# Optimization experiments

Measured on AMD Instinct MI355X. Metric: run time of the kernel, lower is better.

The kernel has to match this reference:

```python
import jax, jax.numpy as jnp
import numpy as np

V_IPC, N_ROLES, D = 50000, 16, 256
B, L = 2048, 64
F_BIB, H1, H2, D_OUT = 512, 1024, 1024, 512
N_EXP, N_CLS = 8, 10
LN_EPS = 1e-5


def setup_inputs() -> dict:
    key = jax.random.key(0)
    ks = jax.random.split(key, 24)
    s = 0.05
    ipc_emb = jax.random.normal(ks[0], (V_IPC, D), jnp.float32) * s
    ipc_emb = ipc_emb.at[0].set(0.0)  # padding_idx=0
    role_emb = jax.random.normal(ks[1], (N_ROLES, D), jnp.float32) * s
    role_emb = role_emb.at[0].set(0.0)
    inp = {
        "ipc_indices": jax.random.randint(ks[2], (B, L), 0, V_IPC),
        "role_indices": jax.random.randint(ks[3], (B, L), 0, N_ROLES),
        "bibliometric_features": jax.random.normal(ks[4], (B, F_BIB), jnp.float32),
        "ipc_padding_mask": jax.random.randint(ks[5], (B, L), 0, 2).astype(jnp.int32),
        "top_k": 2,
        "ipc_emb": ipc_emb,
        "role_emb": role_emb,
        "Wq": jax.random.normal(ks[6], (D, D), jnp.float32) * s,
        "bq": jnp.zeros((D,), jnp.float32),
        "Wk": jax.random.normal(ks[7], (D, D), jnp.float32) * s,
        "bk": jnp.zeros((D,), jnp.float32),
        "Wv": jax.random.normal(ks[8], (D, D), jnp.float32) * s,
        "bv": jnp.zeros((D,), jnp.float32),
        "global_context": jax.random.normal(ks[9], (D,), jnp.float32) * s,
        "ln_g": jnp.ones((D,), jnp.float32),
        "ln_b": jnp.zeros((D,), jnp.float32),
        "gate_W": jax.random.normal(ks[10], (D, N_EXP), jnp.float32) * s,
        "gate_b": jnp.zeros((N_EXP,), jnp.float32),
        "expert_biases": jnp.zeros((N_EXP,), jnp.float32),
        "W1": jax.random.normal(ks[11], (N_EXP, F_BIB, H1), jnp.float32) * s,
        "b1": jnp.zeros((N_EXP, H1), jnp.float32),
        "W2": jax.random.normal(ks[12], (N_EXP, H1, H2), jnp.float32) * s,
        "b2": jnp.zeros((N_EXP, H2), jnp.float32),
        "W3": jax.random.normal(ks[13], (N_EXP, H2, D_OUT), jnp.float32) * s,
        "b3": jnp.zeros((N_EXP, D_OUT), jnp.float32),
        "head_W": jax.random.normal(ks[14], (D_OUT, N_CLS), jnp.float32) * s,
        "head_b": jnp.zeros((N_CLS,), jnp.float32),
    }
    return inp


def reference(ipc_indices, role_indices, bibliometric_features, ipc_padding_mask, top_k,
              ipc_emb, role_emb, Wq, bq, Wk, bk, Wv, bv, global_context, ln_g, ln_b,
              gate_W, gate_b, expert_biases, W1, b1, W2, b2, W3, b3, head_W, head_b):
    # embeddings + role combine  -> [B, L, D]
    x = ipc_emb[ipc_indices] + role_emb[role_indices]
    # attention pooling with a global learned query (same query for every batch row)
    keys = x @ Wk + bk                                  # [B, L, D]
    values = x @ Wv + bv                                # [B, L, D]
    q = global_context @ Wq + bq                        # [D]
    scores = jnp.einsum('d,bld->bl', q, keys)           # [B, L]
    scores = jnp.where(ipc_padding_mask == 0, -1e9, scores)
    attn = jax.nn.softmax(scores, axis=-1)              # [B, L]
    pooled = jnp.einsum('bl,bld->bd', attn, values)     # [B, D]
    mu = pooled.mean(-1, keepdims=True)
    var = ((pooled - mu) ** 2).mean(-1, keepdims=True)
    router_in = (pooled - mu) / jnp.sqrt(var + LN_EPS) * ln_g + ln_b
    # router: select with biased scores, gate with unbiased scores
    affinity = router_in @ gate_W + gate_b              # [B, E]
    sel_scores = affinity + expert_biases
    _, idx = jax.lax.top_k(sel_scores, top_k)           # [B, K]
    gw = jax.nn.softmax(jnp.take_along_axis(affinity, idx, axis=-1), axis=-1)  # [B, K]
    # dense all-expert MLP (reference form of masked per-expert loop)
    h = jax.nn.relu(jnp.einsum('bi,eih->ebh', bibliometric_features, W1) + b1[:, None, :])
    h = jax.nn.relu(jnp.einsum('ebh,ehj->ebj', h, W2) + b2[:, None, :])
    eo = jnp.einsum('ebj,ejo->ebo', h, W3) + b3[:, None, :]  # [E, B, O]
    # gather each token's top-k expert outputs and combine
    bidx = jnp.arange(idx.shape[0])[:, None]            # [B, 1]
    sel_out = eo[idx, bidx]                             # [B, K, O]
    moe_out = jnp.einsum('bk,bko->bo', gw, sel_out)     # [B, O]
    logits = moe_out @ head_W + head_b                  # [B, n_classes]
    return logits, idx
```

## Files before the change

### kernel.cpp

```cpp
#include <hip/hip_runtime.h>
#include <hip/hip_bf16.h>
#include <math.h>


#define LN_EPS 1e-5f

typedef __bf16 bf16_t;
typedef __bf16 bf16x8 __attribute__((ext_vector_type(8)));
typedef float f32x4 __attribute__((ext_vector_type(4)));

struct f4x2 { float4 a, b; };
__device__ __forceinline__ f4x2 ldA8(const float* p) {
  f4x2 v; v.a = *(const float4*)p; v.b = *(const float4*)(p + 4); return v;
}
__device__ __forceinline__ bf16x8 cvt8(const f4x2& v) {
  bf16x8 o;
  o[0] = (bf16_t)v.a.x; o[1] = (bf16_t)v.a.y; o[2] = (bf16_t)v.a.z; o[3] = (bf16_t)v.a.w;
  o[4] = (bf16_t)v.b.x; o[5] = (bf16_t)v.b.y; o[6] = (bf16_t)v.b.z; o[7] = (bf16_t)v.b.w;
  return o;
}

__global__ __launch_bounds__(256)
void prep_kq_kernel(const float* __restrict__ Wq, const float* __restrict__ bq,
                    const float* __restrict__ Wk, const float* __restrict__ bk,
                    const float* __restrict__ gc, float* __restrict__ kq_out,
                    int* __restrict__ done_ctr) {
  __shared__ float q[256];
  __shared__ float red[4];
  const int t = threadIdx.x, bi = blockIdx.x;
  if (bi == 0 && t == 0) *done_ctr = 0;
  float s = bq[t];
  for (int d = 0; d < 256; d++) s += gc[d] * Wq[d * 256 + t];
  q[t] = s;
  __syncthreads();
  const int rl = t >> 5, sl = t & 31;
  const int r = bi * 8 + rl;
  float p = 0.f;
#pragma unroll
  for (int i = 0; i < 8; i++) { const int d = sl + 32 * i; p += Wk[r * 256 + d] * q[d]; }
#pragma unroll
  for (int o = 16; o > 0; o >>= 1) p += __shfl_down(p, o, 32);
  if (sl == 0) kq_out[r] = p;
  if (bi == 0) {
    float z2 = q[t] * bk[t];
    const int lane = t & 63, wave = t >> 6;
#pragma unroll
    for (int o = 32; o > 0; o >>= 1) z2 += __shfl_down(z2, o);
    if (lane == 0) red[wave] = z2;
    __syncthreads();
    if (t == 0) kq_out[256] = red[0] + red[1] + red[2] + red[3];
  }
}

__global__ __launch_bounds__(256, 8)
void xbar_transpose(const float* __restrict__ W1, const float* __restrict__ W2,
                    const float* __restrict__ W3, bf16_t* __restrict__ B1,
                    bf16_t* __restrict__ B2, bf16_t* __restrict__ B3,
                    const int* __restrict__ ipc_idx, const int* __restrict__ role_idx,
                    const int* __restrict__ maskp,
                    const float* __restrict__ ipc_emb, const float* __restrict__ role_emb,
                    const float* __restrict__ kq_qbk, float* __restrict__ xbar_g) {
  __shared__ __align__(16) float smem[4480];
  __shared__ int s_ii[64], s_ri[64], s_mk[64];
  const int bid = blockIdx.x;
  const int t = threadIdx.x, lane = t & 63;

  if (bid < 2048) {
    const int b = bid, wave = t >> 6;
    float* sred = smem;
    float* scores_s = smem + 4352;
    float* attn_s = smem + 4416;
    const float4 kq = *(const float4*)(kq_qbk + lane * 4);
    const float qbk = kq_qbk[256];
    if (t < 64) {
      const int mk = maskp[b * 64 + t];
      s_mk[t] = mk;
      s_ii[t] = mk ? ipc_idx[b * 64 + t] : 0;
      s_ri[t] = mk ? role_idx[b * 64 + t] : 0;
    }
    __syncthreads();
#pragma unroll
    for (int i = 0; i < 16; i++) {
      const int row = wave * 16 + i;
      const int ii = s_ii[row], ri = s_ri[row];
      const float4 xe = *(const float4*)(ipc_emb + (size_t)ii * 256 + lane * 4);
      const float4 re = *(const float4*)(role_emb + (size_t)ri * 256 + lane * 4);
      sred[(wave * 64 + lane) * 17 + i] =
          (xe.x + re.x) * kq.x + (xe.y + re.y) * kq.y +
          (xe.z + re.z) * kq.z + (xe.w + re.w) * kq.w;
    }
    __syncthreads();
    {
      const int i_r = lane & 15, g = lane >> 4;
      float s = 0.f;
#pragma unroll
      for (int j = 0; j < 16; j++) s += sred[(wave * 64 + g * 16 + j) * 17 + i_r];
      s += __shfl_xor(s, 16);
      s += __shfl_xor(s, 32);
      if (lane < 16)
        scores_s[wave * 16 + lane] = s_mk[wave * 16 + lane] ? (s + qbk) : -1e9f;
    }
    __syncthreads();
    if (wave == 0) {
      const float sv = scores_s[lane];
      float m = sv;
#pragma unroll
      for (int o = 32; o > 0; o >>= 1) m = fmaxf(m, __shfl_xor(m, o));
      const float ev = expf(sv - m);
      float sum = ev;
#pragma unroll
      for (int o = 32; o > 0; o >>= 1) sum += __shfl_xor(sum, o);
      attn_s[lane] = ev / sum;
    }
    __syncthreads();
    float p0 = 0.f, p1 = 0.f, p2 = 0.f, p3 = 0.f;
#pragma unroll
    for (int i = 0; i < 16; i++) {
      const int row = wave * 16 + i;
      const int ii = s_ii[row], ri = s_ri[row];
      const float a = attn_s[row];
      const float4 xe = *(const float4*)(ipc_emb + (size_t)ii * 256 + lane * 4);
      const float4 re = *(const float4*)(role_emb + (size_t)ri * 256 + lane * 4);
      p0 += a * (xe.x + re.x); p1 += a * (xe.y + re.y);
      p2 += a * (xe.z + re.z); p3 += a * (xe.w + re.w);
    }
    __syncthreads();
    *(float4*)&smem[wave * 256 + lane * 4] = make_float4(p0, p1, p2, p3);
    __syncthreads();
    xbar_g[(size_t)b * 256 + t] = smem[t] + smem[256 + t] + smem[512 + t] + smem[768 + t];
    return;
  }

  const int bid2 = bid - 2048;
  const float* W; bf16_t* Bft; int K, N, e, n0, k0;
  if (bid2 < 1024) {
    W = W1; Bft = B1; K = 512; N = 1024;
    e = bid2 >> 7; const int r = bid2 & 127;
    n0 = (r & 15) * 64; k0 = (r >> 4) * 64;
  } else if (bid2 < 3072) {
    W = W2; Bft = B2; K = 1024; N = 1024;
    const int q = bid2 - 1024; e = q >> 8; const int r = q & 255;
    n0 = (r & 15) * 64; k0 = (r >> 4) * 64;
  } else {
    W = W3; Bft = B3; K = 1024; N = 512;
    const int q = bid2 - 3072; e = q >> 7; const int r = q & 127;
    n0 = (r & 7) * 64; k0 = (r >> 3) * 64;
  }
  float (*tile)[65] = (float(*)[65])smem;
  const float* Wp = W + (size_t)e * K * N;
  bf16_t* Bp = Bft + (size_t)e * N * K;
  const int tq = t & 15, th = t >> 4;
#pragma unroll
  for (int i = 0; i < 4; i++) {
    const int row = th + 16 * i;
    *(float4*)&tile[row][tq * 4] = *(const float4*)(Wp + (size_t)(k0 + row) * N + n0 + tq * 4);
  }
  __syncthreads();
  const int sub = t >> 6;
  const int nk = K >> 5;
#pragma unroll
  for (int it = 0; it < 2; it++) {
    const int fid = sub + it * 4;
    const int ntl = fid & 3, ktl = fid >> 2;
    const int n_l = ntl * 16 + (lane & 15);
    const int k_l = ktl * 32 + (lane >> 4) * 8;
    bf16x8 o;
#pragma unroll
    for (int j = 0; j < 8; j++) o[j] = (bf16_t)tile[k_l + j][n_l];
    const size_t idx = ((((size_t)(n0 >> 4) + ntl) * nk + (k0 >> 5) + ktl) * 64 + lane) * 8;
    *(bf16x8*)(Bp + idx) = o;
  }
}

__global__ __launch_bounds__(256)
void pool_kernel(const float* __restrict__ xbar_g, const float* __restrict__ Wv,
                 const float* __restrict__ bvec,
                 const float* __restrict__ ln_g, const float* __restrict__ ln_b,
                 const float* __restrict__ gate_W, const float* __restrict__ gate_b,
                 const float* __restrict__ expert_biases,
                 float* __restrict__ out_idx_f, int* __restrict__ ws_idx,
                 float* __restrict__ ws_gw, int* __restrict__ done_ctr,
                 int* __restrict__ list_token, int* __restrict__ a_of,
                 int* __restrict__ offsets_g) {
  const int rb = blockIdx.x * 8;
  __shared__ __align__(16) float xs[8][256];
  __shared__ __align__(16) float pp[4][8][256];
  __shared__ int is_last;
  const int t = threadIdx.x, wave = t >> 6, lane = t & 63;
  for (int i = t; i < 512; i += 256)
    ((float4*)xs)[i] = ((const float4*)(xbar_g + (size_t)rb * 256))[i];
  __syncthreads();
  f32x4 acc[8];
#pragma unroll
  for (int r = 0; r < 8; r++) acc[r] = (f32x4){0.f, 0.f, 0.f, 0.f};
  const int dbase = wave * 64;
  for (int dd = 0; dd < 64; dd += 4) {
    float4 xr[8];
#pragma unroll
    for (int r = 0; r < 8; r++) xr[r] = *(const float4*)&xs[r][dbase + dd];
#pragma unroll
    for (int j = 0; j < 4; j++) {
      const float4 wv = *(const float4*)(Wv + (size_t)(dbase + dd + j) * 256 + lane * 4);
#pragma unroll
      for (int r = 0; r < 8; r++) {
        const float xv = (&xr[r].x)[j];
        acc[r][0] += xv * wv.x; acc[r][1] += xv * wv.y;
        acc[r][2] += xv * wv.z; acc[r][3] += xv * wv.w;
      }
    }
  }
#pragma unroll
  for (int r = 0; r < 8; r++) *(f32x4*)&pp[wave][r][lane * 4] = acc[r];
  __syncthreads();
  const float4 bvv = *(const float4*)(bvec + lane * 4);
  const float4 lg = *(const float4*)(ln_g + lane * 4);
  const float4 lb = *(const float4*)(ln_b + lane * 4);
#pragma unroll
  for (int rr = 0; rr < 2; rr++) {
    const int r = wave * 2 + rr;
    f32x4 v = *(const f32x4*)&pp[0][r][lane * 4];
#pragma unroll
    for (int w2 = 1; w2 < 4; w2++) {
      const f32x4 qv = *(const f32x4*)&pp[w2][r][lane * 4];
      v[0] += qv[0]; v[1] += qv[1]; v[2] += qv[2]; v[3] += qv[3];
    }
    v[0] += bvv.x; v[1] += bvv.y; v[2] += bvv.z; v[3] += bvv.w;
    float s1 = v[0] + v[1] + v[2] + v[3];
#pragma unroll
    for (int o = 32; o > 0; o >>= 1) s1 += __shfl_xor(s1, o);
    const float mu = s1 * (1.f / 256.f);
    const float4 df = make_float4(v[0] - mu, v[1] - mu, v[2] - mu, v[3] - mu);
    float s2 = df.x * df.x + df.y * df.y + df.z * df.z + df.w * df.w;
#pragma unroll
    for (int o = 32; o > 0; o >>= 1) s2 += __shfl_xor(s2, o);
    const float inv = 1.f / sqrtf(s2 * (1.f / 256.f) + LN_EPS);
    f32x4 rv;
    rv[0] = df.x * inv * lg.x + lb.x; rv[1] = df.y * inv * lg.y + lb.y;
    rv[2] = df.z * inv * lg.z + lb.z; rv[3] = df.w * inv * lg.w + lb.w;
    f32x4 pa = {0.f, 0.f, 0.f, 0.f}, pb = {0.f, 0.f, 0.f, 0.f};
#pragma unroll
    for (int k = 0; k < 4; k++) {
      const int d = lane * 4 + k;
      const f32x4 g0 = *(const f32x4*)(gate_W + d * 8);
      const f32x4 g1 = *(const f32x4*)(gate_W + d * 8 + 4);
      pa += rv[k] * g0;
      pb += rv[k] * g1;
    }
#pragma unroll
    for (int o = 32; o > 0; o >>= 1) {
      pa[0] += __shfl_down(pa[0], o); pa[1] += __shfl_down(pa[1], o);
      pa[2] += __shfl_down(pa[2], o); pa[3] += __shfl_down(pa[3], o);
      pb[0] += __shfl_down(pb[0], o); pb[1] += __shfl_down(pb[1], o);
      pb[2] += __shfl_down(pb[2], o); pb[3] += __shfl_down(pb[3], o);
    }
    if (lane == 0) {
      float aff[8];
#pragma unroll
      for (int j = 0; j < 4; j++) { aff[j] = pa[j] + gate_b[j]; aff[4 + j] = pb[j] + gate_b[4 + j]; }
      float b0 = -1e30f; int i0 = 0;
#pragma unroll
      for (int j = 0; j < 8; j++) {
        const float s = aff[j] + expert_biases[j];
        if (s > b0) { b0 = s; i0 = j; }
      }
      float b1v = -1e30f; int i1 = 0;
#pragma unroll
      for (int j = 0; j < 8; j++) {
        const float s = aff[j] + expert_biases[j];
        if (j != i0 && s > b1v) { b1v = s; i1 = j; }
      }
      const float a0 = aff[i0], a1 = aff[i1];
      const float m = fmaxf(a0, a1);
      const float e0 = expf(a0 - m), e1 = expf(a1 - m);
      const float invs = 1.f / (e0 + e1);
      const int bg = rb + r;
      ws_idx[bg * 2] = i0; ws_idx[bg * 2 + 1] = i1;
      ws_gw[bg * 2] = e0 * invs; ws_gw[bg * 2 + 1] = e1 * invs;
      out_idx_f[bg * 2] = (float)i0; out_idx_f[bg * 2 + 1] = (float)i1;
    }
  }
  __syncthreads();
  if (t == 0) {
    __threadfence();
    const int prev = atomicAdd(done_ctr, 1);
    is_last = (prev == (int)gridDim.x - 1);
  }
  __syncthreads();
  if (is_last) {
    __threadfence();
    __shared__ int cnt[8]; __shared__ int offp[9]; __shared__ int fill[8];
    if (t < 8) cnt[t] = 0;
    __syncthreads();
    for (int a = t; a < 4096; a += 256) atomicAdd(&cnt[ws_idx[a]], 1);
    __syncthreads();
    if (t == 0) {
      offp[0] = 0;
      for (int e = 0; e < 8; e++) offp[e + 1] = offp[e] + ((cnt[e] + 63) & ~63);
    }
    __syncthreads();
    if (t < 8) fill[t] = offp[t];
    if (t < 9) offsets_g[t] = offp[t];
    for (int a = t; a < 4608; a += 256) list_token[a] = 0;
    __syncthreads();
    for (int a = t; a < 4096; a += 256) {
      const int e = ws_idx[a];
      const int pos = atomicAdd(&fill[e], 1);
      list_token[pos] = a >> 1;
      a_of[a] = pos;
    }
  }
}

template <int NT, bool RELU>
__global__ __launch_bounds__(256)
void expert_gemm_g1(const float* __restrict__ bib, const int* __restrict__ list_token,
                    const bf16_t* __restrict__ Bft, const float* __restrict__ bias,
                    bf16_t* __restrict__ C, const int* __restrict__ offsets) {
  constexpr int K = 512, nk = K / 32;
  const int e = blockIdx.z;
  const int seg_hi = offsets[e + 1];
  const int blk_row = offsets[e] + blockIdx.y * 128;
  if (blk_row >= seg_hi) return;
  const int wave = threadIdx.x >> 6, lane = threadIdx.x & 63;
  const int row0 = blk_row + wave * 32;
  if (row0 >= seg_hi) return;
  const int n0 = blockIdx.x * 64;
  const int tok0 = list_token[row0 + (lane & 15)];
  const int tok1 = list_token[row0 + 16 + (lane & 15)];
  const float* Ap0 = bib + (size_t)tok0 * 512 + (lane >> 4) * 8;
  const float* Ap1 = bib + (size_t)tok1 * 512 + (lane >> 4) * 8;
  const bf16_t* Bp = Bft + (size_t)e * NT * K + ((size_t)(n0 >> 4) * nk * 512 + lane * 8);
  f32x4 acc[2][4];
#pragma unroll
  for (int i = 0; i < 2; i++)
#pragma unroll
    for (int j = 0; j < 4; j++) acc[i][j] = (f32x4){0.f, 0.f, 0.f, 0.f};
  f4x2 aS[2][2]; bf16x8 bX[2][4];
  aS[0][0] = ldA8(Ap0); aS[0][1] = ldA8(Ap1);
#pragma unroll
  for (int ni = 0; ni < 4; ni++) bX[0][ni] = *(const bf16x8*)(Bp + (size_t)ni * nk * 512);
#pragma unroll
  for (int kt = 0; kt < nk; kt++) {
    const int cur = kt & 1, nxt = cur ^ 1;
    if (kt + 1 < nk) {
      aS[nxt][0] = ldA8(Ap0 + (kt + 1) * 32);
      aS[nxt][1] = ldA8(Ap1 + (kt + 1) * 32);
#pragma unroll
      for (int ni = 0; ni < 4; ni++)
        bX[nxt][ni] = *(const bf16x8*)(Bp + ((size_t)ni * nk + kt + 1) * 512);
    }
    const bf16x8 a0 = cvt8(aS[cur][0]), a1 = cvt8(aS[cur][1]);
#pragma unroll
    for (int ni = 0; ni < 4; ni++) {
      acc[0][ni] = __builtin_amdgcn_mfma_f32_16x16x32_bf16(a0, bX[cur][ni], acc[0][ni], 0, 0, 0);
      acc[1][ni] = __builtin_amdgcn_mfma_f32_16x16x32_bf16(a1, bX[cur][ni], acc[1][ni], 0, 0, 0);
    }
  }
  const int fr = lane & 15, q = lane >> 4;
#pragma unroll
  for (int ni = 0; ni < 4; ni++) {
    const int col = n0 + ni * 16 + fr;
    const float bv = bias[e * NT + col];
#pragma unroll
    for (int mi = 0; mi < 2; mi++) {
#pragma unroll
      for (int r = 0; r < 4; r++) {
        const int row = row0 + mi * 16 + q * 4 + r;
        float v = acc[mi][ni][r] + bv;
        if (RELU) v = fmaxf(v, 0.f);
        C[(size_t)row * NT + col] = (bf16_t)v;
      }
    }
  }
}

template <int K, int NT, bool RELU, typename OUT_T>
__global__ __launch_bounds__(256)
void expert_gemm_ft(const bf16_t* __restrict__ A, const bf16_t* __restrict__ Bft,
                    const float* __restrict__ bias, OUT_T* __restrict__ C,
                    const int* __restrict__ offsets) {
  constexpr int nk = K / 32;
  const int e = blockIdx.z;
  const int seg_hi = offsets[e + 1];
  const int blk_row = offsets[e] + blockIdx.y * 128;
  if (blk_row >= seg_hi) return;
  const int wave = threadIdx.x >> 6, lane = threadIdx.x & 63;
  const int row0 = blk_row + wave * 32;
  if (row0 >= seg_hi) return;
  const int n0 = blockIdx.x * 64;
  const bf16_t* Ap = A + (size_t)(row0 + (lane & 15)) * K + ((lane >> 4) * 8);
  const bf16_t* Bp = Bft + (size_t)e * NT * K + ((size_t)(n0 >> 4) * nk * 512 + lane * 8);
  f32x4 acc[2][4];
#pragma unroll
  for (int i = 0; i < 2; i++)
#pragma unroll
    for (int j = 0; j < 4; j++) acc[i][j] = (f32x4){0.f, 0.f, 0.f, 0.f};
  bf16x8 aX[2][2], bX[2][4];
#pragma unroll
  for (int mi = 0; mi < 2; mi++) aX[0][mi] = *(const bf16x8*)(Ap + mi * 16 * K);
#pragma unroll
  for (int ni = 0; ni < 4; ni++) bX[0][ni] = *(const bf16x8*)(Bp + (size_t)ni * nk * 512);
#pragma unroll
  for (int kt = 0; kt < nk; kt++) {
    const int cur = kt & 1, nxt = cur ^ 1;
    if (kt + 1 < nk) {
#pragma unroll
      for (int mi = 0; mi < 2; mi++)
        aX[nxt][mi] = *(const bf16x8*)(Ap + mi * 16 * K + (kt + 1) * 32);
#pragma unroll
      for (int ni = 0; ni < 4; ni++)
        bX[nxt][ni] = *(const bf16x8*)(Bp + ((size_t)ni * nk + kt + 1) * 512);
    }
#pragma unroll
    for (int mi = 0; mi < 2; mi++)
#pragma unroll
      for (int ni = 0; ni < 4; ni++)
        acc[mi][ni] = __builtin_amdgcn_mfma_f32_16x16x32_bf16(aX[cur][mi], bX[cur][ni], acc[mi][ni], 0, 0, 0);
  }
  const int fr = lane & 15, q = lane >> 4;
#pragma unroll
  for (int ni = 0; ni < 4; ni++) {
    const int col = n0 + ni * 16 + fr;
    const float bv = bias[e * NT + col];
#pragma unroll
    for (int mi = 0; mi < 2; mi++) {
#pragma unroll
      for (int r = 0; r < 4; r++) {
        const int row = row0 + mi * 16 + q * 4 + r;
        float v = acc[mi][ni][r] + bv;
        if (RELU) v = fmaxf(v, 0.f);
        C[(size_t)row * NT + col] = (OUT_T)v;
      }
    }
  }
}

__global__ __launch_bounds__(256)
void head_kernel(const float* __restrict__ O, const int* __restrict__ a_of,
                 const float* __restrict__ ws_gw, const float* __restrict__ head_W,
                 const float* __restrict__ head_b, float* __restrict__ out) {
  const int b = blockIdx.x, t = threadIdx.x;
  __shared__ float m[512];
  const int a0 = a_of[b * 2], a1 = a_of[b * 2 + 1];
  const float g0 = ws_gw[b * 2], g1 = ws_gw[b * 2 + 1];
  for (int d = t; d < 512; d += 256)
    m[d] = g0 * O[(size_t)a0 * 512 + d] + g1 * O[(size_t)a1 * 512 + d];
  __syncthreads();
  if (t < 160) {
    const int c = t >> 4, ch = t & 15;
    float p = 0.f;
#pragma unroll
    for (int i = 0; i < 32; i++) {
      const int d = i * 16 + ch;
      p += m[d] * head_W[d * 10 + c];
    }
#pragma unroll
    for (int o = 8; o > 0; o >>= 1) p += __shfl_down(p, o, 16);
    if (ch == 0) out[b * 10 + c] = p + head_b[c];
  }
}

extern "C" void kernel_launch(void* const* d_in, const int* in_sizes, int n_in,
                              void* d_out, int out_size, void* d_ws, size_t ws_size,
                              hipStream_t stream) {
  const int* ipc_idx = (const int*)d_in[0];
  const int* role_idx = (const int*)d_in[1];
  const float* bib = (const float*)d_in[2];
  const int* maskp = (const int*)d_in[3];
  const float* ipc_emb = (const float*)d_in[5];
  const float* role_emb = (const float*)d_in[6];
  const float* Wq = (const float*)d_in[7];
  const float* bq = (const float*)d_in[8];
  const float* Wk = (const float*)d_in[9];
  const float* bk = (const float*)d_in[10];
  const float* Wv = (const float*)d_in[11];
  const float* bv = (const float*)d_in[12];
  const float* gc = (const float*)d_in[13];
  const float* ln_g = (const float*)d_in[14];
  const float* ln_b = (const float*)d_in[15];
  const float* gate_W = (const float*)d_in[16];
  const float* gate_b = (const float*)d_in[17];
  const float* exp_b = (const float*)d_in[18];
  const float* W1 = (const float*)d_in[19];
  const float* b1 = (const float*)d_in[20];
  const float* W2 = (const float*)d_in[21];
  const float* b2 = (const float*)d_in[22];
  const float* W3 = (const float*)d_in[23];
  const float* b3 = (const float*)d_in[24];
  const float* head_W = (const float*)d_in[25];
  const float* head_b = (const float*)d_in[26];

  char* ws = (char*)d_ws;
  size_t off = 0;
  auto alloc = [&](size_t bytes) -> char* {
    char* p = ws + off;
    off += (bytes + 255) & ~(size_t)255;
    return p;
  };
  float* kq_qbk = (float*)alloc(257 * 4);
  float* xbar_g = (float*)alloc((size_t)2048 * 256 * 4);
  int* ws_idx = (int*)alloc(4096 * 4);
  float* ws_gw = (float*)alloc(4096 * 4);
  int* list_tok = (int*)alloc(4608 * 4);
  int* a_of = (int*)alloc(4096 * 4);
  int* offs = (int*)alloc(9 * 4);
  int* done_ctr = (int*)alloc(4);
  bf16_t* W1t = (bf16_t*)alloc((size_t)8 * 1024 * 512 * 2);
  bf16_t* W2t = (bf16_t*)alloc((size_t)8 * 1024 * 1024 * 2);
  bf16_t* W3t = (bf16_t*)alloc((size_t)8 * 512 * 1024 * 2);
  bf16_t* H1c = (bf16_t*)alloc((size_t)4608 * 1024 * 2);
  bf16_t* H2c = (bf16_t*)alloc((size_t)4608 * 1024 * 2);
  float* Oc = (float*)alloc((size_t)4608 * 512 * 4);
  (void)in_sizes; (void)n_in; (void)out_size; (void)ws_size;

  float* out_logits = (float*)d_out;
  float* out_idx = (float*)d_out + 20480;

  prep_kq_kernel<<<32, 256, 0, stream>>>(Wq, bq, Wk, bk, gc, kq_qbk, done_ctr);
  xbar_transpose<<<6144, 256, 0, stream>>>(W1, W2, W3, W1t, W2t, W3t,
                                           ipc_idx, role_idx, maskp,
                                           ipc_emb, role_emb, kq_qbk, xbar_g);
  pool_kernel<<<256, 256, 0, stream>>>(xbar_g, Wv, bv, ln_g, ln_b, gate_W, gate_b,
                                       exp_b, out_idx, ws_idx, ws_gw,
                                       done_ctr, list_tok, a_of, offs);
  expert_gemm_g1<1024, true><<<dim3(16, 36, 8), 256, 0, stream>>>(bib, list_tok, W1t, b1, H1c, offs);
  expert_gemm_ft<1024, 1024, true, bf16_t><<<dim3(16, 36, 8), 256, 0, stream>>>(H1c, W2t, b2, H2c, offs);
  expert_gemm_ft<1024, 512, false, float><<<dim3(8, 36, 8), 256, 0, stream>>>(H2c, W3t, b3, Oc, offs);
  head_kernel<<<2048, 256, 0, stream>>>(Oc, a_of, ws_gw, head_W, head_b, out_logits);
}
```

Measured before the change: 365.8 us.

## Fold head projection into W3 so the last expert GEMM outputs ten logits

Precomputes W3·head_W and b3·head_W per expert (padded to 16 columns, stored as bf16 in MFMA fragment layout). The third expert GEMM therefore produces 16 columns instead of 512, and the head kernel becomes a tiny gated combine. This removes most of the layer-3 GEMM FLOPs, the large fp32 Oc buffer and the W3 transpose. Separately, the pooling blocks now load mask and index values straight into registers with vector loads instead of staging them in shared memory. The trade-off is extra rounding, since the folded weights are cast to bf16, and a serial per-class reduction inside the prep blocks.

```diff
diff --git a/kernel.cpp b/kernel.cpp
--- a/kernel.cpp
+++ b/kernel.cpp
@@ -52,16 +52,17 @@
   }
 }
 
-__global__ __launch_bounds__(256, 8)
+__global__ __launch_bounds__(256)
 void xbar_transpose(const float* __restrict__ W1, const float* __restrict__ W2,
                     const float* __restrict__ W3, bf16_t* __restrict__ B1,
-                    bf16_t* __restrict__ B2, bf16_t* __restrict__ B3,
+                    bf16_t* __restrict__ B2, bf16_t* __restrict__ B3h,
+                    float* __restrict__ b3h_g,
+                    const float* __restrict__ b3, const float* __restrict__ head_W,
                     const int* __restrict__ ipc_idx, const int* __restrict__ role_idx,
                     const int* __restrict__ maskp,
                     const float* __restrict__ ipc_emb, const float* __restrict__ role_emb,
                     const float* __restrict__ kq_qbk, float* __restrict__ xbar_g) {
   __shared__ __align__(16) float smem[4480];
-  __shared__ int s_ii[64], s_ri[64], s_mk[64];
   const int bid = blockIdx.x;
   const int t = threadIdx.x, lane = t & 63;
 
@@ -72,17 +73,19 @@
     float* attn_s = smem + 4416;
     const float4 kq = *(const float4*)(kq_qbk + lane * 4);
     const float qbk = kq_qbk[256];
-    if (t < 64) {
-      const int mk = maskp[b * 64 + t];
-      s_mk[t] = mk;
-      s_ii[t] = mk ? ipc_idx[b * 64 + t] : 0;
-      s_ri[t] = mk ? role_idx[b * 64 + t] : 0;
-    }
-    __syncthreads();
+    const int rbase = b * 64 + wave * 16;
+    int4 m4[4], i4[4], r4[4];
+#pragma unroll
+    for (int j = 0; j < 4; j++) {
+      m4[j] = *(const int4*)(maskp + rbase + j * 4);
+      i4[j] = *(const int4*)(ipc_idx + rbase + j * 4);
+      r4[j] = *(const int4*)(role_idx + rbase + j * 4);
+    }
 #pragma unroll
     for (int i = 0; i < 16; i++) {
-      const int row = wave * 16 + i;
-      const int ii = s_ii[row], ri = s_ri[row];
+      const int mki = (&m4[i / 4].x)[i % 4];
+      const int ii = mki ? (&i4[i / 4].x)[i % 4] : 0;
+      const int ri = mki ? (&r4[i / 4].x)[i % 4] : 0;
       const float4 xe = *(const float4*)(ipc_emb + (size_t)ii * 256 + lane * 4);
       const float4 re = *(const float4*)(role_emb + (size_t)ri * 256 + lane * 4);
       sred[(wave * 64 + lane) * 17 + i] =
@@ -97,8 +100,8 @@
       for (int j = 0; j < 16; j++) s += sred[(wave * 64 + g * 16 + j) * 17 + i_r];
       s += __shfl_xor(s, 16);
       s += __shfl_xor(s, 32);
-      if (lane < 16)
-        scores_s[wave * 16 + lane] = s_mk[wave * 16 + lane] ? (s + qbk) : -1e9f;
+      const int mval = (&m4[i_r / 4].x)[i_r % 4];
+      if (lane < 16) scores_s[wave * 16 + lane] = mval ? (s + qbk) : -1e9f;
     }
     __syncthreads();
     if (wave == 0) {
@@ -116,9 +119,10 @@
     float p0 = 0.f, p1 = 0.f, p2 = 0.f, p3 = 0.f;
 #pragma unroll
     for (int i = 0; i < 16; i++) {
-      const int row = wave * 16 + i;
-      const int ii = s_ii[row], ri = s_ri[row];
-      const float a = attn_s[row];
+      const int mki = (&m4[i / 4].x)[i % 4];
+      const int ii = mki ? (&i4[i / 4].x)[i % 4] : 0;
+      const int ri = mki ? (&r4[i / 4].x)[i % 4] : 0;
+      const float a = attn_s[wave * 16 + i];
       const float4 xe = *(const float4*)(ipc_emb + (size_t)ii * 256 + lane * 4);
       const float4 re = *(const float4*)(role_emb + (size_t)ri * 256 + lane * 4);
       p0 += a * (xe.x + re.x); p1 += a * (xe.y + re.y);
@@ -132,19 +136,60 @@
   }
 
   const int bid2 = bid - 2048;
+  if (bid2 >= 3072) {
+    const int q = bid2 - 3072;
+    const int e = q >> 5, kt = q & 31;
+    const int wave = t >> 6;
+    float* w3h_s = smem;
+    for (int i = t; i < 32 * 16; i += 256) w3h_s[i] = 0.f;
+    __syncthreads();
+    const int ob = lane * 8;
+#pragma unroll
+    for (int r = 0; r < 8; r++) {
+      const int kl = wave * 8 + r;
+      const int k = kt * 32 + kl;
+      const f4x2 wv = ldA8(W3 + ((size_t)e * 1024 + k) * 512 + ob);
+      for (int c = 0; c < 10; c++) {
+        float p = wv.a.x * head_W[(ob + 0) * 10 + c] + wv.a.y * head_W[(ob + 1) * 10 + c] +
+                  wv.a.z * head_W[(ob + 2) * 10 + c] + wv.a.w * head_W[(ob + 3) * 10 + c] +
+                  wv.b.x * head_W[(ob + 4) * 10 + c] + wv.b.y * head_W[(ob + 5) * 10 + c] +
+                  wv.b.z * head_W[(ob + 6) * 10 + c] + wv.b.w * head_W[(ob + 7) * 10 + c];
+#pragma unroll
+        for (int o = 32; o > 0; o >>= 1) p += __shfl_down(p, o);
+        if (lane == 0) w3h_s[kl * 16 + c] = p;
+      }
+    }
+    __syncthreads();
+    if (wave == 0) {
+      bf16x8 o8;
+      const int n_l = lane & 15, k_l = (lane >> 4) * 8;
+#pragma unroll
+      for (int j = 0; j < 8; j++) o8[j] = (bf16_t)w3h_s[(k_l + j) * 16 + n_l];
+      *(bf16x8*)(B3h + (size_t)e * 16 * 1024 + ((size_t)kt * 64 + lane) * 8) = o8;
+    }
+    if (kt == 0 && wave == 1) {
+      for (int c = 0; c < 10; c++) {
+        float p = 0.f;
+#pragma unroll
+        for (int j = 0; j < 8; j++) p += b3[e * 512 + ob + j] * head_W[(ob + j) * 10 + c];
+#pragma unroll
+        for (int o = 32; o > 0; o >>= 1) p += __shfl_down(p, o);
+        if (lane == 0) b3h_g[e * 16 + c] = p;
+      }
+      if (lane >= 10 && lane < 16) b3h_g[e * 16 + lane] = 0.f;
+    }
+    return;
+  }
+
   const float* W; bf16_t* Bft; int K, N, e, n0, k0;
   if (bid2 < 1024) {
     W = W1; Bft = B1; K = 512; N = 1024;
     e = bid2 >> 7; const int r = bid2 & 127;
     n0 = (r & 15) * 64; k0 = (r >> 4) * 64;
-  } else if (bid2 < 3072) {
+  } else {
     W = W2; Bft = B2; K = 1024; N = 1024;
     const int q = bid2 - 1024; e = q >> 8; const int r = q & 255;
     n0 = (r & 15) * 64; k0 = (r >> 4) * 64;
-  } else {
-    W = W3; Bft = B3; K = 1024; N = 512;
-    const int q = bid2 - 3072; e = q >> 7; const int r = q & 127;
-    n0 = (r & 7) * 64; k0 = (r >> 3) * 64;
   }
   float (*tile)[65] = (float(*)[65])smem;
   const float* Wp = W + (size_t)e * K * N;
@@ -374,7 +419,7 @@
   }
 }
 
-template <int K, int NT, bool RELU, typename OUT_T>
+template <int K, int NT, int NFRAG, bool RELU, typename OUT_T>
 __global__ __launch_bounds__(256)
 void expert_gemm_ft(const bf16_t* __restrict__ A, const bf16_t* __restrict__ Bft,
                     const float* __restrict__ bias, OUT_T* __restrict__ C,
@@ -387,19 +432,19 @@
   const int wave = threadIdx.x >> 6, lane = threadIdx.x & 63;
   const int row0 = blk_row + wave * 32;
   if (row0 >= seg_hi) return;
-  const int n0 = blockIdx.x * 64;
+  const int n0 = blockIdx.x * (16 * NFRAG);
   const bf16_t* Ap = A + (size_t)(row0 + (lane & 15)) * K + ((lane >> 4) * 8);
   const bf16_t* Bp = Bft + (size_t)e * NT * K + ((size_t)(n0 >> 4) * nk * 512 + lane * 8);
-  f32x4 acc[2][4];
+  f32x4 acc[2][NFRAG];
 #pragma unroll
   for (int i = 0; i < 2; i++)
 #pragma unroll
-    for (int j = 0; j < 4; j++) acc[i][j] = (f32x4){0.f, 0.f, 0.f, 0.f};
-  bf16x8 aX[2][2], bX[2][4];
+    for (int j = 0; j < NFRAG; j++) acc[i][j] = (f32x4){0.f, 0.f, 0.f, 0.f};
+  bf16x8 aX[2][2], bX[2][NFRAG];
 #pragma unroll
   for (int mi = 0; mi < 2; mi++) aX[0][mi] = *(const bf16x8*)(Ap + mi * 16 * K);
 #pragma unroll
-  for (int ni = 0; ni < 4; ni++) bX[0][ni] = *(const bf16x8*)(Bp + (size_t)ni * nk * 512);
+  for (int ni = 0; ni < NFRAG; ni++) bX[0][ni] = *(const bf16x8*)(Bp + (size_t)ni * nk * 512);
 #pragma unroll
   for (int kt = 0; kt < nk; kt++) {
     const int cur = kt & 1, nxt = cur ^ 1;
@@ -408,18 +453,18 @@
       for (int mi = 0; mi < 2; mi++)
         aX[nxt][mi] = *(const bf16x8*)(Ap + mi * 16 * K + (kt + 1) * 32);
 #pragma unroll
-      for (int ni = 0; ni < 4; ni++)
+      for (int ni = 0; ni < NFRAG; ni++)
         bX[nxt][ni] = *(const bf16x8*)(Bp + ((size_t)ni * nk + kt + 1) * 512);
     }
 #pragma unroll
     for (int mi = 0; mi < 2; mi++)
 #pragma unroll
-      for (int ni = 0; ni < 4; ni++)
+      for (int ni = 0; ni < NFRAG; ni++)
         acc[mi][ni] = __builtin_amdgcn_mfma_f32_16x16x32_bf16(aX[cur][mi], bX[cur][ni], acc[mi][ni], 0, 0, 0);
   }
   const int fr = lane & 15, q = lane >> 4;
 #pragma unroll
-  for (int ni = 0; ni < 4; ni++) {
+  for (int ni = 0; ni < NFRAG; ni++) {
     const int col = n0 + ni * 16 + fr;
     const float bv = bias[e * NT + col];
 #pragma unroll
@@ -436,28 +481,15 @@
 }
 
 __global__ __launch_bounds__(256)
-void head_kernel(const float* __restrict__ O, const int* __restrict__ a_of,
-                 const float* __restrict__ ws_gw, const float* __restrict__ head_W,
-                 const float* __restrict__ head_b, float* __restrict__ out) {
-  const int b = blockIdx.x, t = threadIdx.x;
-  __shared__ float m[512];
+void head_small(const float* __restrict__ OcH, const int* __restrict__ a_of,
+                const float* __restrict__ ws_gw, const float* __restrict__ head_b,
+                float* __restrict__ out) {
+  const int tid = blockIdx.x * 256 + threadIdx.x;
+  if (tid >= 20480) return;
+  const int b = tid / 10, c = tid - b * 10;
   const int a0 = a_of[b * 2], a1 = a_of[b * 2 + 1];
   const float g0 = ws_gw[b * 2], g1 = ws_gw[b * 2 + 1];
-  for (int d = t; d < 512; d += 256)
-    m[d] = g0 * O[(size_t)a0 * 512 + d] + g1 * O[(size_t)a1 * 512 + d];
-  __syncthreads();
-  if (t < 160) {
-    const int c = t >> 4, ch = t & 15;
-    float p = 0.f;
-#pragma unroll
-    for (int i = 0; i < 32; i++) {
-      const int d = i * 16 + ch;
-      p += m[d] * head_W[d * 10 + c];
-    }
-#pragma unroll
-    for (int o = 8; o > 0; o >>= 1) p += __shfl_down(p, o, 16);
-    if (ch == 0) out[b * 10 + c] = p + head_b[c];
-  }
+  out[tid] = g0 * OcH[(size_t)a0 * 16 + c] + g1 * OcH[(size_t)a1 * 16 + c] + head_b[c];
 }
 
 extern "C" void kernel_launch(void* const* d_in, const int* in_sizes, int n_in,
@@ -505,26 +537,28 @@
   int* a_of = (int*)alloc(4096 * 4);
   int* offs = (int*)alloc(9 * 4);
   int* done_ctr = (int*)alloc(4);
+  float* b3h = (float*)alloc(8 * 16 * 4);
   bf16_t* W1t = (bf16_t*)alloc((size_t)8 * 1024 * 512 * 2);
   bf16_t* W2t = (bf16_t*)alloc((size_t)8 * 1024 * 1024 * 2);
-  bf16_t* W3t = (bf16_t*)alloc((size_t)8 * 512 * 1024 * 2);
+  bf16_t* B3h = (bf16_t*)alloc((size_t)8 * 16 * 1024 * 2);
   bf16_t* H1c = (bf16_t*)alloc((size_t)4608 * 1024 * 2);
   bf16_t* H2c = (bf16_t*)alloc((size_t)4608 * 1024 * 2);
-  float* Oc = (float*)alloc((size_t)4608 * 512 * 4);
+  float* OcH = (float*)alloc((size_t)4608 * 16 * 4);
   (void)in_sizes; (void)n_in; (void)out_size; (void)ws_size;
 
   float* out_logits = (float*)d_out;
   float* out_idx = (float*)d_out + 20480;
 
   prep_kq_kernel<<<32, 256, 0, stream>>>(Wq, bq, Wk, bk, gc, kq_qbk, done_ctr);
-  xbar_transpose<<<6144, 256, 0, stream>>>(W1, W2, W3, W1t, W2t, W3t,
+  xbar_transpose<<<5376, 256, 0, stream>>>(W1, W2, W3, W1t, W2t, B3h, b3h,
+                                           b3, head_W,
                                            ipc_idx, role_idx, maskp,
                                            ipc_emb, role_emb, kq_qbk, xbar_g);
   pool_kernel<<<256, 256, 0, stream>>>(xbar_g, Wv, bv, ln_g, ln_b, gate_W, gate_b,
                                        exp_b, out_idx, ws_idx, ws_gw,
                                        done_ctr, list_tok, a_of, offs);
   expert_gemm_g1<1024, true><<<dim3(16, 36, 8), 256, 0, stream>>>(bib, list_tok, W1t, b1, H1c, offs);
-  expert_gemm_ft<1024, 1024, true, bf16_t><<<dim3(16, 36, 8), 256, 0, stream>>>(H1c, W2t, b2, H2c, offs);
-  expert_gemm_ft<1024, 512, false, float><<<dim3(8, 36, 8), 256, 0, stream>>>(H2c, W3t, b3, Oc, offs);
-  head_kernel<<<2048, 256, 0, stream>>>(Oc, a_of, ws_gw, head_W, head_b, out_logits);
-}
+  expert_gemm_ft<1024, 1024, 4, true, bf16_t><<<dim3(16, 36, 8), 256, 0, stream>>>(H1c, W2t, b2, H2c, offs);
+  expert_gemm_ft<1024, 16, 1, false, float><<<dim3(1, 36, 8), 256, 0, stream>>>(H2c, B3h, b3h, OcH, offs);
+  head_small<<<80, 256, 0, stream>>>(OcH, a_of, ws_gw, head_b, out_logits);
+}
```

Result: slower. 381.6 us (+4.3%).
